# Kernel tuning notes

Measured on AMD Instinct MI355X. Metric: run time of the kernel, lower is better.

Reference implementation:

```python
import math
import jax, jax.numpy as jnp
import numpy as np

D_MODEL, N_HEADS, D_HEAD, D_INNER = 512, 8, 64, 2048
QLEN, MLEN, BATCH = 2048, 2048, 2


def _layernorm(x, g, b, eps=1e-5):
    mu = jnp.mean(x, axis=-1, keepdims=True)
    var = jnp.var(x, axis=-1, keepdims=True)
    return (x - mu) * jax.lax.rsqrt(var + eps) * g + b


def _rel_shift(x):
    # x: [qlen, klen, B, n] -> Transformer-XL relative shift
    q, k, b, n = x.shape
    x = jnp.pad(x, ((0, 0), (1, 0), (0, 0), (0, 0)))  # zero-pad key dim at front
    x = x.reshape(k + 1, q, b, n)[1:].reshape(q, k, b, n)
    return x


def setup_inputs() -> dict:
    key = jax.random.key(0)
    ks = jax.random.split(key, 16)
    nd = N_HEADS * D_HEAD
    s = 0.02
    return {
        "x": jax.random.normal(ks[0], (QLEN, BATCH, D_MODEL), jnp.float32),
        "r": jax.random.normal(ks[1], (QLEN + MLEN, D_MODEL), jnp.float32),
        "u": jax.random.normal(ks[2], (N_HEADS, D_HEAD), jnp.float32) * s,
        "v": jax.random.normal(ks[3], (N_HEADS, D_HEAD), jnp.float32) * s,
        "mems": jax.random.normal(ks[4], (MLEN, BATCH, D_MODEL), jnp.float32),
        "Wqkv": jax.random.normal(ks[5], (3 * nd, D_MODEL), jnp.float32) * s,
        "Wr": jax.random.normal(ks[6], (nd, D_MODEL), jnp.float32) * s,
        "Wo": jax.random.normal(ks[7], (D_MODEL, nd), jnp.float32) * s,
        "ln1_g": jnp.ones((D_MODEL,), jnp.float32),
        "ln1_b": jnp.zeros((D_MODEL,), jnp.float32),
        "W1": jax.random.normal(ks[8], (D_MODEL, D_INNER), jnp.float32) * s,
        "b1": jnp.zeros((D_INNER,), jnp.float32),
        "W2": jax.random.normal(ks[9], (D_INNER, D_MODEL), jnp.float32) * s,
        "b2": jnp.zeros((D_MODEL,), jnp.float32),
        "ln2_g": jnp.ones((D_MODEL,), jnp.float32),
        "ln2_b": jnp.zeros((D_MODEL,), jnp.float32),
    }


def reference(x, r, u, v, mems, Wqkv, Wr, Wo, ln1_g, ln1_b, W1, b1, W2, b2, ln2_g, ln2_b):
    qlen, B, d_model = x.shape
    n_heads, d_head = u.shape
    cat = jnp.concatenate([mems, x], axis=0)          # [klen, B, d_model]
    klen = cat.shape[0]
    mlen = klen - qlen

    qkv = cat @ Wqkv.T                                 # [klen, B, 3*n*d]
    q, k, val = jnp.split(qkv, 3, axis=-1)
    q = q[-qlen:].reshape(qlen, B, n_heads, d_head)
    k = k.reshape(klen, B, n_heads, d_head)
    val = val.reshape(klen, B, n_heads, d_head)
    rk = (r @ Wr.T).reshape(klen, n_heads, d_head)     # relative key heads

    AC = jnp.einsum('ibnd,jbnd->ijbn', q + u, k)       # content score
    BD = _rel_shift(jnp.einsum('ibnd,jnd->ijbn', q + v, rk))  # position score
    score = (AC + BD) * (1.0 / math.sqrt(d_head))      # [qlen, klen, B, n]

    # causal mask with memory: query i attends keys j <= i + mlen
    mask = jnp.arange(klen)[None, :] > (jnp.arange(qlen)[:, None] + mlen)
    score = jnp.where(mask[:, :, None, None], jnp.float32(-1e30), score)
    attn = jax.nn.softmax(score, axis=1)

    out = jnp.einsum('ijbn,jbnd->ibnd', attn, val).reshape(qlen, B, n_heads * d_head)
    out = out @ Wo.T
    h = _layernorm(x + out, ln1_g, ln1_b)              # post-LN attention

    core = jax.nn.relu(h @ W1 + b1) @ W2 + b2          # PositionwiseFF
    return _layernorm(h + core, ln2_g, ln2_b)
```

## Files before the change

kernel.cpp:

```cpp
#include <hip/hip_runtime.h>
#include <hip/hip_bf16.h>

#define QLEN 2048
#define MLEN 2048
#define KLEN 4096
#define BATCH 2
#define DMODEL 512
#define NHEADS 8
#define DHEAD 64
#define DINNER 2048

typedef __attribute__((ext_vector_type(8))) short  vs8;
typedef __attribute__((ext_vector_type(8))) __bf16 vbf8;
typedef __attribute__((ext_vector_type(4))) float  vf4;

__device__ __forceinline__ float bf2f(ushort h) {
    union { unsigned u; float f; } c; c.u = ((unsigned)h) << 16; return c.f;
}
__device__ __forceinline__ ushort f2bf(float f) {
    return __builtin_bit_cast(unsigned short, (__bf16)f);
}
__device__ __forceinline__ unsigned cvtpk(float lo, float hi) {
    unsigned r;
    asm("v_cvt_pk_bf16_f32 %0, %1, %2" : "=v"(r) : "v"(lo), "v"(hi));
    return r;
}
__device__ __forceinline__ vf4 mfma16(vs8 a, vs8 b, vf4 c) {
    return __builtin_amdgcn_mfma_f32_16x16x32_bf16(
        __builtin_bit_cast(vbf8, a), __builtin_bit_cast(vbf8, b), c, 0, 0, 0);
}
__device__ __forceinline__ void gl16(const ushort* g, ushort* l) {
    __builtin_amdgcn_global_load_lds(
        (const __attribute__((address_space(1))) void*)g,
        (__attribute__((address_space(3))) void*)l, 16, 0, 0);
}
#define WAITV4 asm volatile("s_waitcnt vmcnt(4)" ::: "memory")
#define WAITV0 asm volatile("s_waitcnt vmcnt(0)" ::: "memory")
__device__ __forceinline__ void barx() {
    asm volatile("" ::: "memory");
    __builtin_amdgcn_s_barrier();
    asm volatile("" ::: "memory");
}

__global__ void cvt_bf(const float* __restrict__ in, ushort* __restrict__ out, int nel4) {
    int i = blockIdx.x * 256 + threadIdx.x;
    if (i < nel4) {
        float4 f = ((const float4*)in)[i];
        ushort4 o; o.x = f2bf(f.x); o.y = f2bf(f.y); o.z = f2bf(f.z); o.w = f2bf(f.w);
        ((ushort4*)out)[i] = o;
    }
}

__global__ void cvt_cat(const float* __restrict__ mems, const float* __restrict__ x,
                        ushort* __restrict__ out) {
    int i = blockIdx.x * 256 + threadIdx.x;
    const int half4 = MLEN * BATCH * DMODEL / 4;
    if (i < 2 * half4) {
        float4 f = (i < half4) ? ((const float4*)mems)[i] : ((const float4*)x)[i - half4];
        ushort4 o; o.x = f2bf(f.x); o.y = f2bf(f.y); o.z = f2bf(f.z); o.w = f2bf(f.w);
        ((ushort4*)out)[i] = o;
    }
}

__global__ void cvt_tr(const float* __restrict__ in, ushort* __restrict__ out, int R, int C) {
    __shared__ float t[32][33];
    const int c0 = blockIdx.x * 32, r0 = blockIdx.y * 32;
    const int tx = threadIdx.x & 31, ty = threadIdx.x >> 5;
#pragma unroll
    for (int q = 0; q < 4; ++q) {
        int r = ty + q * 8;
        t[r][tx] = in[(size_t)(r0 + r) * C + c0 + tx];
    }
    __syncthreads();
#pragma unroll
    for (int q = 0; q < 4; ++q) {
        int c = ty + q * 8;
        out[(size_t)(c0 + c) * R + r0 + tx] = f2bf(t[tx][c]);
    }
}

__global__ void vtrans(const ushort* __restrict__ qkv, ushort* __restrict__ vT) {
    __shared__ __align__(16) ushort t_lds[64][72];
    const int j0 = blockIdx.x * 64, n = blockIdx.y, b = blockIdx.z;
    const int tid = threadIdx.x;
#pragma unroll
    for (int p = 0; p < 2; ++p) {
        int u2 = p * 256 + tid;
        int j = u2 >> 3, d8 = (u2 & 7) * 8;
        vs8 v8 = *(const vs8*)(qkv + ((size_t)(j0 + j) * BATCH + b) * 1536 + 1024 + n * 64 + d8);
#pragma unroll
        for (int e = 0; e < 8; ++e) t_lds[d8 + e][j] = (ushort)v8[e];
    }
    __syncthreads();
#pragma unroll
    for (int p = 0; p < 2; ++p) {
        int u2 = p * 256 + tid;
        int d = u2 >> 3, j8 = (u2 & 7) * 8;
        vs8 o8 = *(const vs8*)&t_lds[d][j8];
        *(vs8*)(vT + ((size_t)(b * NHEADS + n) * 64 + d) * KLEN + j0 + j8) = o8;
    }
}

template <int EPI>
__global__ __launch_bounds__(256)
void gemm_bt(const ushort* __restrict__ A, const ushort* __restrict__ B,
             void* __restrict__ C0, void* __restrict__ C1,
             const float* __restrict__ bias, int M, int N, int K, int kc, int ldc) {
    __shared__ __align__(16) ushort As[2][128 * 32];
    __shared__ __align__(16) ushort Bs[2][128 * 32];
    const int n0 = blockIdx.x * 128;
    const int m0 = blockIdx.y * 128;
    const int kb = blockIdx.z * kc;
    void* C = blockIdx.z ? C1 : C0;
    const int tid = threadIdx.x;
    const int lane = tid & 63, wave = tid >> 6;
    const int wr = wave >> 1, wc = wave & 1;
    const int lr = lane & 15, lg = lane >> 4;
    vf4 acc[4][4] = {};

    auto stage = [&](int bi, int k0) {
#pragma unroll
        for (int t = 0; t < 2; ++t) {
            int u = t * 256 + tid;
            int row = u >> 2, cu = u & 3;
            int sc = cu ^ ((row >> 1) & 3);
            gl16(&A[(size_t)(m0 + row) * K + k0 + sc * 8],
                 &As[bi][t * 2048 + (tid & 192) * 8]);
            gl16(&B[(size_t)(n0 + row) * K + k0 + sc * 8],
                 &Bs[bi][t * 2048 + (tid & 192) * 8]);
        }
    };

    const int nt = kc >> 5;
    stage(0, kb);
    int cur = 0;
    for (int t = 0; t < nt; ++t) {
        if (t + 1 < nt) { stage(cur ^ 1, kb + (t + 1) * 32); WAITV4; }
        else { WAITV0; }
        barx();
        vs8 af[4], bfr[4];
#pragma unroll
        for (int m = 0; m < 4; ++m) {
            int rr = wr * 64 + m * 16 + lr;
            af[m] = *(const vs8*)&As[cur][rr * 32 + (lg ^ ((rr >> 1) & 3)) * 8];
        }
#pragma unroll
        for (int nn = 0; nn < 4; ++nn) {
            int rr = wc * 64 + nn * 16 + lr;
            bfr[nn] = *(const vs8*)&Bs[cur][rr * 32 + (lg ^ ((rr >> 1) & 3)) * 8];
        }
#pragma unroll
        for (int m = 0; m < 4; ++m)
#pragma unroll
            for (int nn = 0; nn < 4; ++nn)
                acc[m][nn] = mfma16(af[m], bfr[nn], acc[m][nn]);
        barx();
        cur ^= 1;
    }

#pragma unroll
    for (int m = 0; m < 4; ++m) {
#pragma unroll
        for (int nn = 0; nn < 4; ++nn) {
            int row0 = m0 + wr * 64 + m * 16 + lg * 4;
            int col  = n0 + wc * 64 + nn * 16 + lr;
#pragma unroll
            for (int rr = 0; rr < 4; ++rr) {
                float vv = acc[m][nn][rr];
                size_t off = (size_t)(row0 + rr) * ldc + col;
                if (EPI == 0) ((float*)C)[off] = vv;
                else if (EPI == 1) ((ushort*)C)[off] = f2bf(vv);
                else if (EPI == 2) {
                    float t2 = vv + bias[col];
                    ((ushort*)C)[off] = f2bf(t2 > 0.f ? t2 : 0.f);
                } else {
                    ((ushort*)C)[(((size_t)(col >> 6)) << 18) + (size_t)(row0 + rr) * 64 + (col & 63)]
                        = f2bf(vv);
                }
            }
        }
    }
}

__global__ __launch_bounds__(256, 3)
void attn2(const ushort* __restrict__ qkv, const ushort* __restrict__ rkh,
           const ushort* __restrict__ vT, const float* __restrict__ uu,
           const float* __restrict__ vv, float* __restrict__ part_l,
           ushort* __restrict__ part_o) {
    __shared__ __align__(16) ushort K_lds[64 * 64];
    __shared__ __align__(16) ushort V_lds[64 * 64];
    __shared__ __align__(16) ushort w_lds[4][16 * 84];

    const int chunk = blockIdx.x & 1, qb = 31 - (blockIdx.x >> 1);
    const int b = blockIdx.y, n = blockIdx.z;
    const int tid = threadIdx.x, lane = tid & 63, w = tid >> 6;
    const int lr = lane & 15, lg = lane >> 4;
    const int i0w = qb * 64 + w * 16;

    ushort* wl = w_lds[w];
    const ushort* rh  = rkh + ((size_t)n << 18);
    const ushort* vTh = vT + (size_t)(b * NHEADS + n) * 64 * KLEN;

    const float S = 0.18033688011112042f;
    vs8 aqu[2], aqv[2];
#pragma unroll
    for (int kk = 0; kk < 2; ++kk) {
        int d0 = kk * 32 + lg * 8;
        vs8 q8 = *(const vs8*)(qkv + ((size_t)(i0w + lr + MLEN) * BATCH + b) * 1536 + n * 64 + d0);
#pragma unroll
        for (int e = 0; e < 8; ++e) {
            float qf = bf2f((ushort)q8[e]);
            aqu[kk][e] = (short)f2bf((qf + uu[n * 64 + d0 + e]) * S);
            aqv[kk][e] = (short)f2bf((qf + vv[n * 64 + d0 + e]) * S);
        }
    }

    const vf4 zero4 = {0.f, 0.f, 0.f, 0.f};
    vf4 o[4] = {zero4, zero4, zero4, zero4};
    float l_run = 0.f;

    const int jstart = chunk * 2048;
    int avail = qb * 64 + 2111 - jstart;
    int niter = avail < 0 ? 0 : (avail >> 6) + 1;
    niter = niter > 32 ? 32 : niter;

    const int slot = lane & 7;
    vs8 kreg[2], vreg[2];
    auto ldkv = [&](int j0) {
#pragma unroll
        for (int p2 = 0; p2 < 2; ++p2) {
            int row = p2 * 32 + w * 8 + (lane >> 3);
            int g = (slot - row) & 7;
            kreg[p2] = *(const vs8*)(qkv + ((size_t)(j0 + row) * BATCH + b) * 1536 + 512 + n * 64 + g * 8);
            vreg[p2] = *(const vs8*)(vTh + (size_t)row * KLEN + j0 + g * 8);
        }
    };
    auto wrkv = [&]() {
#pragma unroll
        for (int p2 = 0; p2 < 2; ++p2) {
            int row = p2 * 32 + w * 8 + (lane >> 3);
            *(vs8*)&K_lds[row * 64 + slot * 8] = kreg[p2];
            *(vs8*)&V_lds[row * 64 + slot * 8] = vreg[p2];
        }
    };

    ldkv(jstart);
    wrkv();
    __syncthreads();
    for (int it = 0; it < niter; ++it) {
        const int j0 = jstart + it * 64;
        const bool more = (it + 1 < niter);
        if (more) ldkv(j0 + 64);

        vf4 acc_s[4] = {zero4, zero4, zero4, zero4};
#pragma unroll
        for (int jg = 0; jg < 4; ++jg) {
            int jr = jg * 16 + lr;
#pragma unroll
            for (int kk = 0; kk < 2; ++kk) {
                vs8 kb = *(const vs8*)&K_lds[jr * 64 + ((kk * 4 + lg + jr) & 7) * 8];
                acc_s[jg] = mfma16(kb, aqu[kk], acc_s[jg]);
            }
        }
        const int mbase = j0 - i0w + 2032;
#pragma unroll
        for (int wg = 0; wg < 5; ++wg) {
            vf4 aw = zero4;
            int mrow = mbase + wg * 16 + lr;
            mrow = mrow > KLEN - 1 ? KLEN - 1 : mrow;
#pragma unroll
            for (int kk = 0; kk < 2; ++kk) {
                vs8 rb = *(const vs8*)(rh + (size_t)mrow * 64 + kk * 32 + lg * 8);
                aw = mfma16(rb, aqv[kk], aw);
            }
#pragma unroll
            for (int r = 0; r < 4; ++r)
                wl[lr * 84 + wg * 16 + lg * 4 + r] = f2bf(aw[r]);
        }

        const int thr = i0w + 2048 - j0;
        const int bw = lr * 83 + 15;
        if (thr >= 63) {
#pragma unroll
            for (int jg = 0; jg < 4; ++jg)
#pragma unroll
                for (int r = 0; r < 4; ++r) {
                    float p4 = __builtin_amdgcn_exp2f(
                        acc_s[jg][r] + bf2f(wl[bw + jg * 16 + lg * 4 + r]));
                    acc_s[jg][r] = p4;
                    l_run += p4;
                }
        } else {
#pragma unroll
            for (int jg = 0; jg < 4; ++jg)
#pragma unroll
                for (int r = 0; r < 4; ++r) {
                    int jrel = jg * 16 + lg * 4 + r;
                    float p4 = (jrel - lr > thr) ? 0.f
                        : __builtin_amdgcn_exp2f(
                              acc_s[jg][r] + bf2f(wl[bw + jg * 16 + lg * 4 + r]));
                    acc_s[jg][r] = p4;
                    l_run += p4;
                }
        }

        unsigned pw0[4], pw1[4];
#pragma unroll
        for (int jg = 0; jg < 4; ++jg) {
            pw0[jg] = cvtpk(acc_s[jg][0], acc_s[jg][1]);
            pw1[jg] = cvtpk(acc_s[jg][2], acc_s[jg][3]);
        }

        const int srcA = (lg & 1) * 32 + lr, srcB = srcA + 16;
        const bool hi = (lg >> 1) != 0;
#pragma unroll
        for (int kk = 0; kk < 2; ++kk) {
            unsigned a0 = __shfl(pw0[2 * kk], srcA), b0 = __shfl(pw0[2 * kk + 1], srcA);
            unsigned a1 = __shfl(pw1[2 * kk], srcA), b1 = __shfl(pw1[2 * kk + 1], srcA);
            unsigned a2 = __shfl(pw0[2 * kk], srcB), b2 = __shfl(pw0[2 * kk + 1], srcB);
            unsigned a3 = __shfl(pw1[2 * kk], srcB), b3 = __shfl(pw1[2 * kk + 1], srcB);
            int4 pu = { (int)(hi ? b0 : a0), (int)(hi ? b1 : a1),
                        (int)(hi ? b2 : a2), (int)(hi ? b3 : a3) };
            vs8 pfrag = __builtin_bit_cast(vs8, pu);
#pragma unroll
            for (int dg = 0; dg < 4; ++dg) {
                int dr = dg * 16 + lr;
                vs8 vfr = *(const vs8*)&V_lds[dr * 64 + ((kk * 4 + lg + dr) & 7) * 8];
                o[dg] = mfma16(vfr, pfrag, o[dg]);
            }
        }
        __syncthreads();
        if (more) { wrkv(); __syncthreads(); }
    }

    float l1 = l_run + __shfl_xor(l_run, 16);
    float l_tot = l1 + __shfl_xor(l1, 32);

#pragma unroll
    for (int dg = 0; dg < 4; ++dg) {
        uint2 uu2 = { cvtpk(o[dg][0], o[dg][1]), cvtpk(o[dg][2], o[dg][3]) };
        *(uint2*)&wl[lr * 68 + dg * 16 + lg * 4] = uu2;
    }
    const int q2 = lane >> 2, dp = (lane & 3) * 16;
    const int i2 = i0w + q2;
    size_t gbase = ((size_t)chunk * 32768 + ((size_t)(i2 * 2 + b) * 8 + n)) * 64 + dp;
    vs8 r0 = *(const vs8*)&wl[q2 * 68 + dp];
    vs8 r1 = *(const vs8*)&wl[q2 * 68 + dp + 8];
    *(vs8*)&part_o[gbase] = r0;
    *(vs8*)&part_o[gbase + 8] = r1;
    if (lg == 0)
        part_l[chunk * 32768 + ((i0w + lr) * 2 + b) * 8 + n] = l_tot;
}

__global__ __launch_bounds__(256)
void combine(const float* __restrict__ part_l, const ushort* __restrict__ part_o,
             ushort* __restrict__ ao) {
    int t = blockIdx.x * 256 + threadIdx.x;
    int pr = t >> 3, d8 = (t & 7) * 8;
    float rl = 1.f / (part_l[pr] + part_l[32768 + pr]);
    vs8 a = *(const vs8*)&part_o[(size_t)pr * 64 + d8];
    vs8 c = *(const vs8*)&part_o[(size_t)(32768 + pr) * 64 + d8];
    vs8 ov;
#pragma unroll
    for (int e = 0; e < 8; ++e)
        ov[e] = (short)f2bf((bf2f((ushort)a[e]) + bf2f((ushort)c[e])) * rl);
    int i2b = pr >> 3, n = pr & 7;
    *(vs8*)(ao + (size_t)i2b * 512 + n * 64 + d8) = ov;
}

__global__ __launch_bounds__(256)
void ln_fuse(const float* __restrict__ base, const float* __restrict__ pa,
             const float* __restrict__ pb, const float* __restrict__ bias,
             const float* __restrict__ g, const float* __restrict__ bb,
             float* __restrict__ of32, ushort* __restrict__ obf) {
    const int row = blockIdx.x * 4 + (threadIdx.x >> 6);
    const int lane = threadIdx.x & 63;
    const size_t off0 = (size_t)row * DMODEL + lane * 8;
    float vals[8];
    float s = 0.f, s2 = 0.f;
#pragma unroll
    for (int e = 0; e < 8; ++e) {
        float t = base[off0 + e] + pa[off0 + e];
        if (pb) t += pb[off0 + e];
        if (bias) t += bias[lane * 8 + e];
        vals[e] = t; s += t; s2 += t * t;
    }
#pragma unroll
    for (int o = 1; o < 64; o <<= 1) { s += __shfl_xor(s, o); s2 += __shfl_xor(s2, o); }
    const float mean = s * (1.f / DMODEL);
    const float var = s2 * (1.f / DMODEL) - mean * mean;
    const float rstd = rsqrtf(var + 1e-5f);
#pragma unroll
    for (int e = 0; e < 8; ++e) {
        int c = lane * 8 + e;
        float y = (vals[e] - mean) * rstd * g[c] + bb[c];
        if (of32) of32[(size_t)row * DMODEL + c] = y;
        if (obf)  obf[(size_t)row * DMODEL + c] = f2bf(y);
    }
}

extern "C" void kernel_launch(void* const* d_in, const int* in_sizes, int n_in,
                              void* d_out, int out_size, void* d_ws, size_t ws_size,
                              hipStream_t stream) {
    const float* x    = (const float*)d_in[0];
    const float* r    = (const float*)d_in[1];
    const float* u    = (const float*)d_in[2];
    const float* v    = (const float*)d_in[3];
    const float* mems = (const float*)d_in[4];
    const float* Wqkv = (const float*)d_in[5];
    const float* Wr   = (const float*)d_in[6];
    const float* Wo   = (const float*)d_in[7];
    const float* ln1g = (const float*)d_in[8];
    const float* ln1b = (const float*)d_in[9];
    const float* W1   = (const float*)d_in[10];
    const float* b1   = (const float*)d_in[11];
    const float* W2   = (const float*)d_in[12];
    const float* b2   = (const float*)d_in[13];
    const float* ln2g = (const float*)d_in[14];
    const float* ln2b = (const float*)d_in[15];
    float* out = (float*)d_out;

    char* p = (char*)d_ws;
    auto alloc = [&](size_t bytes) { char* q = p; p += (bytes + 255) & ~(size_t)255; return q; };
    const size_t MB84 = (size_t)QLEN * BATCH * 512 * 4;
    ushort* cat_bf  = (ushort*)alloc((size_t)KLEN * BATCH * DMODEL * 2);
    ushort* wqkv_bf = (ushort*)alloc((size_t)1536 * 512 * 2);
    ushort* r_bf    = (ushort*)alloc((size_t)KLEN * 512 * 2);
    ushort* wr_bf   = (ushort*)alloc((size_t)512 * 512 * 2);
    ushort* wo_bf   = (ushort*)alloc((size_t)512 * 512 * 2);
    ushort* w1t_bf  = (ushort*)alloc((size_t)DINNER * 512 * 2);
    ushort* w2t_bf  = (ushort*)alloc((size_t)512 * DINNER * 2);
    ushort* qkv_bf  = (ushort*)alloc((size_t)KLEN * BATCH * 1536 * 2);
    ushort* rkh_bf  = (ushort*)alloc((size_t)KLEN * 512 * 2);
    ushort* vT      = (ushort*)alloc((size_t)BATCH * NHEADS * 64 * KLEN * 2);
    ushort* ao_bf   = (ushort*)alloc((size_t)QLEN * BATCH * 512 * 2);
    ushort* h_bf    = (ushort*)alloc((size_t)QLEN * BATCH * 512 * 2);
    float*  part_l  = (float*)alloc((size_t)2 * 32768 * 4);
    char*   big     = alloc(5 * MB84);
    ushort* part_o  = (ushort*)big;
    float*  proj1a  = (float*)big;
    float*  proj1b  = (float*)(big + MB84);
    float*  h_f32   = (float*)(big + 2 * MB84);
    ushort* ff1_bf  = (ushort*)(big + 3 * MB84);
    float*  proj2a  = proj1a;
    float*  proj2b  = proj1b;

    const int MROWS = QLEN * BATCH;
    const int CATROWS = KLEN * BATCH;

    cvt_cat<<<(CATROWS * DMODEL / 4 + 255) / 256, 256, 0, stream>>>(mems, x, cat_bf);
    cvt_bf<<<(KLEN * 512 / 4 + 255) / 256, 256, 0, stream>>>(r, r_bf, KLEN * 512 / 4);
    cvt_bf<<<(1536 * 512 / 4 + 255) / 256, 256, 0, stream>>>(Wqkv, wqkv_bf, 1536 * 512 / 4);
    cvt_bf<<<(512 * 512 / 4 + 255) / 256, 256, 0, stream>>>(Wr, wr_bf, 512 * 512 / 4);
    cvt_bf<<<(512 * 512 / 4 + 255) / 256, 256, 0, stream>>>(Wo, wo_bf, 512 * 512 / 4);
    cvt_tr<<<dim3(DINNER / 32, 512 / 32), 256, 0, stream>>>(W1, w1t_bf, 512, DINNER);
    cvt_tr<<<dim3(512 / 32, DINNER / 32), 256, 0, stream>>>(W2, w2t_bf, DINNER, 512);

    gemm_bt<1><<<dim3(1024 / 128, CATROWS / 128, 1), 256, 0, stream>>>(
        cat_bf, wqkv_bf + (size_t)512 * 512, qkv_bf + 512, nullptr, nullptr,
        CATROWS, 1024, 512, 512, 1536);
    gemm_bt<1><<<dim3(512 / 128, 4096 / 128, 1), 256, 0, stream>>>(
        cat_bf + (size_t)4096 * 512, wqkv_bf, qkv_bf + (size_t)4096 * 1536, nullptr, nullptr,
        4096, 512, 512, 512, 1536);
    gemm_bt<3><<<dim3(512 / 128, KLEN / 128, 1), 256, 0, stream>>>(
        r_bf, wr_bf, rkh_bf, nullptr, nullptr, KLEN, 512, 512, 512, 512);

    vtrans<<<dim3(KLEN / 64, NHEADS, BATCH), 256, 0, stream>>>(qkv_bf, vT);
    attn2<<<dim3(64, BATCH, NHEADS), 256, 0, stream>>>(qkv_bf, rkh_bf, vT, u, v, part_l, part_o);
    combine<<<32768 * 8 / 256, 256, 0, stream>>>(part_l, part_o, ao_bf);

    gemm_bt<0><<<dim3(512 / 128, MROWS / 128, 2), 256, 0, stream>>>(
        ao_bf, wo_bf, proj1a, proj1b, nullptr, MROWS, 512, 512, 256, 512);
    ln_fuse<<<MROWS / 4, 256, 0, stream>>>(x, proj1a, proj1b, nullptr, ln1g, ln1b, h_f32, h_bf);

    gemm_bt<2><<<dim3(DINNER / 128, MROWS / 128, 1), 256, 0, stream>>>(
        h_bf, w1t_bf, ff1_bf, nullptr, b1, MROWS, DINNER, 512, 512, 2048);
    gemm_bt<0><<<dim3(512 / 128, MROWS / 128, 2), 256, 0, stream>>>(
        ff1_bf, w2t_bf, proj2a, proj2b, nullptr, MROWS, 512, 2048, 1024, 512);
    ln_fuse<<<MROWS / 4, 256, 0, stream>>>(h_f32, proj2a, proj2b, b2, ln2g, ln2b, out, nullptr);
}
```

Baseline: 373.0 us.

## Split attention keys across waves per 16-query block, reduce in LDS

Replaces the 64-query-per-block attention kernel, which split the keys into two chunks, with a kernel where each block owns 16 queries and its four waves take interleaved 64-key tiles. K and V fragments are read straight from global memory instead of being staged through LDS with block-wide barriers. Partial outputs and row sums are combined with LDS atomics inside the block, which removes the separate combine kernel and its global partial buffers. Block indices are remapped so that each XCD handles a fixed batch-head pair, aiming for L2 locality. In exchange, K/V reuse across queries now depends on cache hits instead of shared memory, and the final reduction adds atomic traffic.

New measurement: 468.8 us. +25.7%, slower.

```diff
diff --git a/kernel.cpp b/kernel.cpp
--- a/kernel.cpp
+++ b/kernel.cpp
@@ -183,30 +183,37 @@
 }
 
 __global__ __launch_bounds__(256, 3)
-void attn2(const ushort* __restrict__ qkv, const ushort* __restrict__ rkh,
+void attn3(const ushort* __restrict__ qkv, const ushort* __restrict__ rkh,
            const ushort* __restrict__ vT, const float* __restrict__ uu,
-           const float* __restrict__ vv, float* __restrict__ part_l,
-           ushort* __restrict__ part_o) {
-    __shared__ __align__(16) ushort K_lds[64 * 64];
-    __shared__ __align__(16) ushort V_lds[64 * 64];
+           const float* __restrict__ vv, ushort* __restrict__ ao) {
     __shared__ __align__(16) ushort w_lds[4][16 * 84];
-
-    const int chunk = blockIdx.x & 1, qb = 31 - (blockIdx.x >> 1);
-    const int b = blockIdx.y, n = blockIdx.z;
+    __shared__ float obuf[16][65];
+    __shared__ float lbuf[16];
+
+    const int d = blockIdx.x;
+    const int xcd = d & 7, k = d >> 3;
+    const int bn = xcd + 8 * (k >> 7);
+    const int qg = 127 - (k & 127);
+    const int b = bn >> 3, n = bn & 7;
+    const int i0 = qg * 16;
+
     const int tid = threadIdx.x, lane = tid & 63, w = tid >> 6;
     const int lr = lane & 15, lg = lane >> 4;
-    const int i0w = qb * 64 + w * 16;
 
     ushort* wl = w_lds[w];
     const ushort* rh  = rkh + ((size_t)n << 18);
     const ushort* vTh = vT + (size_t)(b * NHEADS + n) * 64 * KLEN;
 
+    if (tid < 16) lbuf[tid] = 0.f;
+    for (int z = tid; z < 16 * 65; z += 256) ((float*)obuf)[z] = 0.f;
+    barx();
+
     const float S = 0.18033688011112042f;
     vs8 aqu[2], aqv[2];
 #pragma unroll
     for (int kk = 0; kk < 2; ++kk) {
         int d0 = kk * 32 + lg * 8;
-        vs8 q8 = *(const vs8*)(qkv + ((size_t)(i0w + lr + MLEN) * BATCH + b) * 1536 + n * 64 + d0);
+        vs8 q8 = *(const vs8*)(qkv + ((size_t)(i0 + lr + MLEN) * BATCH + b) * 1536 + n * 64 + d0);
 #pragma unroll
         for (int e = 0; e < 8; ++e) {
             float qf = bf2f((ushort)q8[e]);
@@ -219,50 +226,22 @@
     vf4 o[4] = {zero4, zero4, zero4, zero4};
     float l_run = 0.f;
 
-    const int jstart = chunk * 2048;
-    int avail = qb * 64 + 2111 - jstart;
-    int niter = avail < 0 ? 0 : (avail >> 6) + 1;
-    niter = niter > 32 ? 32 : niter;
-
-    const int slot = lane & 7;
-    vs8 kreg[2], vreg[2];
-    auto ldkv = [&](int j0) {
-#pragma unroll
-        for (int p2 = 0; p2 < 2; ++p2) {
-            int row = p2 * 32 + w * 8 + (lane >> 3);
-            int g = (slot - row) & 7;
-            kreg[p2] = *(const vs8*)(qkv + ((size_t)(j0 + row) * BATCH + b) * 1536 + 512 + n * 64 + g * 8);
-            vreg[p2] = *(const vs8*)(vTh + (size_t)row * KLEN + j0 + g * 8);
-        }
-    };
-    auto wrkv = [&]() {
-#pragma unroll
-        for (int p2 = 0; p2 < 2; ++p2) {
-            int row = p2 * 32 + w * 8 + (lane >> 3);
-            *(vs8*)&K_lds[row * 64 + slot * 8] = kreg[p2];
-            *(vs8*)&V_lds[row * 64 + slot * 8] = vreg[p2];
-        }
-    };
-
-    ldkv(jstart);
-    wrkv();
-    __syncthreads();
-    for (int it = 0; it < niter; ++it) {
-        const int j0 = jstart + it * 64;
-        const bool more = (it + 1 < niter);
-        if (more) ldkv(j0 + 64);
+    const int nt = ((i0 + 2063) >> 6) + 1;
+    for (int t = w; t < nt; t += 4) {
+        const int j0 = t * 64;
 
         vf4 acc_s[4] = {zero4, zero4, zero4, zero4};
 #pragma unroll
         for (int jg = 0; jg < 4; ++jg) {
-            int jr = jg * 16 + lr;
+            int jr = j0 + jg * 16 + lr;
 #pragma unroll
             for (int kk = 0; kk < 2; ++kk) {
-                vs8 kb = *(const vs8*)&K_lds[jr * 64 + ((kk * 4 + lg + jr) & 7) * 8];
+                vs8 kb = *(const vs8*)(qkv + ((size_t)jr * BATCH + b) * 1536 + 512
+                                       + n * 64 + kk * 32 + lg * 8);
                 acc_s[jg] = mfma16(kb, aqu[kk], acc_s[jg]);
             }
         }
-        const int mbase = j0 - i0w + 2032;
+        const int mbase = j0 - i0 + 2032;
 #pragma unroll
         for (int wg = 0; wg < 5; ++wg) {
             vf4 aw = zero4;
@@ -278,7 +257,7 @@
                 wl[lr * 84 + wg * 16 + lg * 4 + r] = f2bf(aw[r]);
         }
 
-        const int thr = i0w + 2048 - j0;
+        const int thr = i0 + 2048 - j0;
         const int bw = lr * 83 + 15;
         if (thr >= 63) {
 #pragma unroll
@@ -325,47 +304,30 @@
 #pragma unroll
             for (int dg = 0; dg < 4; ++dg) {
                 int dr = dg * 16 + lr;
-                vs8 vfr = *(const vs8*)&V_lds[dr * 64 + ((kk * 4 + lg + dr) & 7) * 8];
+                vs8 vfr = *(const vs8*)(vTh + (size_t)dr * KLEN + j0 + kk * 32 + lg * 8);
                 o[dg] = mfma16(vfr, pfrag, o[dg]);
             }
         }
-        __syncthreads();
-        if (more) { wrkv(); __syncthreads(); }
-    }
-
-    float l1 = l_run + __shfl_xor(l_run, 16);
-    float l_tot = l1 + __shfl_xor(l1, 32);
-
-#pragma unroll
-    for (int dg = 0; dg < 4; ++dg) {
-        uint2 uu2 = { cvtpk(o[dg][0], o[dg][1]), cvtpk(o[dg][2], o[dg][3]) };
-        *(uint2*)&wl[lr * 68 + dg * 16 + lg * 4] = uu2;
-    }
-    const int q2 = lane >> 2, dp = (lane & 3) * 16;
-    const int i2 = i0w + q2;
-    size_t gbase = ((size_t)chunk * 32768 + ((size_t)(i2 * 2 + b) * 8 + n)) * 64 + dp;
-    vs8 r0 = *(const vs8*)&wl[q2 * 68 + dp];
-    vs8 r1 = *(const vs8*)&wl[q2 * 68 + dp + 8];
-    *(vs8*)&part_o[gbase] = r0;
-    *(vs8*)&part_o[gbase + 8] = r1;
-    if (lg == 0)
-        part_l[chunk * 32768 + ((i0w + lr) * 2 + b) * 8 + n] = l_tot;
-}
-
-__global__ __launch_bounds__(256)
-void combine(const float* __restrict__ part_l, const ushort* __restrict__ part_o,
-             ushort* __restrict__ ao) {
-    int t = blockIdx.x * 256 + threadIdx.x;
-    int pr = t >> 3, d8 = (t & 7) * 8;
-    float rl = 1.f / (part_l[pr] + part_l[32768 + pr]);
-    vs8 a = *(const vs8*)&part_o[(size_t)pr * 64 + d8];
-    vs8 c = *(const vs8*)&part_o[(size_t)(32768 + pr) * 64 + d8];
-    vs8 ov;
-#pragma unroll
-    for (int e = 0; e < 8; ++e)
-        ov[e] = (short)f2bf((bf2f((ushort)a[e]) + bf2f((ushort)c[e])) * rl);
-    int i2b = pr >> 3, n = pr & 7;
-    *(vs8*)(ao + (size_t)i2b * 512 + n * 64 + d8) = ov;
+    }
+
+#pragma unroll
+    for (int dg = 0; dg < 4; ++dg)
+#pragma unroll
+        for (int r = 0; r < 4; ++r)
+            atomicAdd(&obuf[lr][dg * 16 + lg * 4 + r], o[dg][r]);
+    atomicAdd(&lbuf[lr], l_run);
+    barx();
+
+    {
+        const int q = tid >> 4, d4 = (tid & 15) * 4;
+        float rl = 1.f / lbuf[q];
+        ushort4 res;
+        res.x = f2bf(obuf[q][d4 + 0] * rl);
+        res.y = f2bf(obuf[q][d4 + 1] * rl);
+        res.z = f2bf(obuf[q][d4 + 2] * rl);
+        res.w = f2bf(obuf[q][d4 + 3] * rl);
+        *(ushort4*)&ao[((size_t)((i0 + q) * 2 + b)) * 512 + n * 64 + d4] = res;
+    }
 }
 
 __global__ __launch_bounds__(256)
@@ -435,9 +397,7 @@
     ushort* vT      = (ushort*)alloc((size_t)BATCH * NHEADS * 64 * KLEN * 2);
     ushort* ao_bf   = (ushort*)alloc((size_t)QLEN * BATCH * 512 * 2);
     ushort* h_bf    = (ushort*)alloc((size_t)QLEN * BATCH * 512 * 2);
-    float*  part_l  = (float*)alloc((size_t)2 * 32768 * 4);
-    char*   big     = alloc(5 * MB84);
-    ushort* part_o  = (ushort*)big;
+    char*   big     = alloc(4 * MB84);
     float*  proj1a  = (float*)big;
     float*  proj1b  = (float*)(big + MB84);
     float*  h_f32   = (float*)(big + 2 * MB84);
@@ -466,8 +426,7 @@
         r_bf, wr_bf, rkh_bf, nullptr, nullptr, KLEN, 512, 512, 512, 512);
 
     vtrans<<<dim3(KLEN / 64, NHEADS, BATCH), 256, 0, stream>>>(qkv_bf, vT);
-    attn2<<<dim3(64, BATCH, NHEADS), 256, 0, stream>>>(qkv_bf, rkh_bf, vT, u, v, part_l, part_o);
-    combine<<<32768 * 8 / 256, 256, 0, stream>>>(part_l, part_o, ao_bf);
+    attn3<<<2048, 256, 0, stream>>>(qkv_bf, rkh_bf, vT, u, v, ao_bf);
 
     gemm_bt<0><<<dim3(512 / 128, MROWS / 128, 2), 256, 0, stream>>>(
         ao_bf, wo_bf, proj1a, proj1b, nullptr, MROWS, 512, 512, 256, 512);
```
